# Optimization experiments

Hardware: AMD Instinct MI355X
Metric: run time of the kernel (lower is better)

## Reference

```python
import jax, jax.numpy as jnp
import numpy as np

# Device/group constants for group_idx = 0 (from the source)
V_REF = 0.25
G_MIN = 1.0 / 983.3
G_MAX = 1.0 / 281.3
N_AVG = 2.132
N_STD = 0.095

P, N_IN, N_OUT = 1024, 784, 128


def setup_inputs() -> dict:
    key = jax.random.key(0)
    k1, k2, k3, k4, k5, k6 = jax.random.split(key, 6)
    x = jax.random.uniform(k1, (P, N_IN), dtype=jnp.float32)  # normalized pixel-like inputs in [0,1)
    stdv = 1.0 / np.sqrt(N_IN)
    w_pos = 0.5 + stdv * jax.random.normal(k2, (N_IN, N_OUT), dtype=jnp.float32)
    w_neg = 0.5 + stdv * jax.random.normal(k3, (N_IN, N_OUT), dtype=jnp.float32)
    b_pos = 0.5 * jnp.ones((N_OUT,), dtype=jnp.float32)
    b_neg = 0.5 * jnp.ones((N_OUT,), dtype=jnp.float32)
    # per-device nonlinearity parameter n ~ N(n_avg, n_std), crossbar shape (m, 2*n_out)
    n_param = N_AVG + N_STD * jax.random.normal(k4, (N_IN + 1, 2 * N_OUT), dtype=jnp.float32)
    return {"x": x, "w_pos": w_pos, "w_neg": w_neg, "b_pos": b_pos, "b_neg": b_neg, "n_param": n_param}


def reference(x, w_pos, w_neg, b_pos, b_neg, n_param):
    # --- build combined (weights+bias row), pos/neg column-interleaved crossbar params ---
    cw_pos = jnp.concatenate([w_pos, b_pos[None, :]], axis=0)  # (m, n_out), m = n_in+1
    cw_neg = jnp.concatenate([w_neg, b_neg[None, :]], axis=0)  # (m, n_out)
    m = cw_pos.shape[0]
    weights = jnp.stack([cw_pos, cw_neg], axis=-1).reshape(m, -1)  # (m, 2*n_out), interleaved

    max_weight = jnp.max(jnp.abs(weights))
    # w_params_to_G: linear map of nonnegative weight params onto [G_min, G_max]
    G = G_MIN + (G_MAX - G_MIN) * weights / max_weight  # (m, 2n)

    # x_to_V with appended ones column (bias word line)
    k_V = 2.0 * V_REF
    ones = jnp.ones((x.shape[0], 1), dtype=x.dtype)
    inputs = jnp.concatenate([x, ones], axis=1)  # (p, m)
    V = k_V * inputs  # (p, m)

    # nonlinear IV: I(V) = sign(V) * G*V_ref * n ** log2(|V|/V_ref)
    exponent = jnp.log2(jnp.maximum(jnp.abs(V), 1e-12) / V_REF)  # (p, m)
    I_ind = jnp.sign(V)[:, :, None] * (V_REF * G)[None, :, :] * n_param[None, :, :] ** exponent[:, :, None]  # (p, m, 2n)
    I = jnp.sum(I_ind, axis=1)  # bit-line currents, (p, 2n)

    # I_to_y: differential pos-neg columns, undo conductance/voltage scaling
    I_total = I[:, 0::2] - I[:, 1::2]  # (p, n_out)
    y = I_total * (max_weight / (k_V * (G_MAX - G_MIN)))
    return y
```

## Files before the change

kernel.cpp:

```cpp
#include <hip/hip_runtime.h>
#include <hip/hip_bf16.h>

#define P_ROWS   1024
#define N_IN     784
#define N_OUT    128
#define M_ROWS   785
#define M_PAD    816
#define OUT_ELEMS (P_ROWS * N_OUT)

#define RATIO_F  ((float)((1.0/983.3) / ((1.0/281.3) - (1.0/983.3))))
#define L_AVG_F  1.0922076f
#define LN2_F    0.6931472f

#define NCH      12
#define CHUNK    68
#define NB_MAIN  (64 * NCH)

#define NB_MAX   32

#define PART_OFF 0
#define C_OFF    256

typedef _Float16 half4 __attribute__((ext_vector_type(4)));

__global__ __launch_bounds__(256) void max_reduce(
        const float* __restrict__ wp, const float* __restrict__ wn,
        const float* __restrict__ bp, const float* __restrict__ bn,
        float* __restrict__ partial) {
    const int b = blockIdx.x, t = threadIdx.x;
    const int nW = N_IN * N_OUT;
    int gid = b * 256 + t;
    float v = 0.0f;
    if (gid < N_OUT) v = fmaxf(fabsf(bp[gid]), fabsf(bn[gid]));
    for (int i = gid; i < nW; i += NB_MAX * 256)
        v = fmaxf(v, fmaxf(fabsf(wp[i]), fabsf(wn[i])));
    for (int off = 32; off > 0; off >>= 1)
        v = fmaxf(v, __shfl_down(v, off, 64));
    __shared__ float smax[4];
    if ((t & 63) == 0) smax[t >> 6] = v;
    __syncthreads();
    if (t == 0)
        partial[b] = fmaxf(fmaxf(smax[0], smax[1]), fmaxf(smax[2], smax[3]));
}

__global__ __launch_bounds__(256) void precompute_c(
        const float* __restrict__ wp, const float* __restrict__ wn,
        const float* __restrict__ bp, const float* __restrict__ bn,
        const float* __restrict__ np, const float* __restrict__ partial,
        half4* __restrict__ C) {
    float mw = 0.0f;
    #pragma unroll
    for (int i = 0; i < NB_MAX; ++i) mw = fmaxf(mw, partial[i]);
    const float c0 = 0.5f * RATIO_F * mw;

    int idx = blockIdx.x * 256 + threadIdx.x;
    int m = idx >> 7, k = idx & 127;
    half4 c = {0.0f16, 0.0f16, 0.0f16, 0.0f16};
    if (m < M_ROWS) {
        float wpv = (m < N_IN) ? wp[m * N_OUT + k] : bp[k];
        float wnv = (m < N_IN) ? wn[m * N_OUT + k] : bn[k];
        float npv = np[m * (2 * N_OUT) + 2 * k];
        float nnv = np[m * (2 * N_OUT) + 2 * k + 1];
        float Dp = LN2_F * (__builtin_amdgcn_logf(npv) - L_AVG_F);
        float Dn = LN2_F * (__builtin_amdgcn_logf(nnv) - L_AVG_F);
        float Ap = c0 + 0.5f * wpv;
        float An = c0 + 0.5f * wnv;
        float ApD = Ap * Dp, AnD = An * Dn;
        float ApD2 = ApD * Dp, AnD2 = AnD * Dn;
        float ApD3 = ApD2 * Dp, AnD3 = AnD2 * Dn;
        c.x = (_Float16)(Ap - An);
        c.y = (_Float16)(ApD - AnD);
        c.z = (_Float16)((ApD2 - AnD2) * 0.5f);
        c.w = (_Float16)((ApD3 - AnD3) * (1.0f / 6.0f));
    }
    C[idx] = c;
}

__global__ __launch_bounds__(256) void memristor_main(
        const float* __restrict__ x, const half4* __restrict__ C,
        float* __restrict__ out) {
    const int bid = blockIdx.x;
    const int ch  = bid % NCH;
    const int pb  = bid / NCH;
    const int p0  = pb * 16;
    const int m0  = ch * CHUNK;
    const int t   = threadIdx.x;

    __shared__ __align__(16) float4 F_lds[16 * CHUNK];
    for (int idx = t; idx < 16 * CHUNK; idx += 256) {
        const int r  = idx / CHUNK;
        const int mm = idx - r * CHUNK;
        const int m  = m0 + mm;
        float e;
        if (m < N_IN) {
            float xv = x[(size_t)(p0 + r) * N_IN + m];
            e = (xv > 0.0f) ? __builtin_amdgcn_logf(2.0f * xv) : -1.0e4f;
        } else {
            e = (m == N_IN) ? 1.0f : -1.0e4f;
        }
        float F0 = __builtin_amdgcn_exp2f(e * L_AVG_F);
        float F1 = F0 * e;
        float F2 = F1 * e;
        float F3 = F2 * e;
        F_lds[r * CHUNK + mm] = make_float4(F0, F1, F2, F3);
    }
    __syncthreads();

    const int lane = t & 63;
    const int wid  = t >> 6;
    const int kh   = wid & 1;
    const int pg   = wid >> 1;
    const int k    = kh * 64 + lane;

    const half4*  __restrict__ Cp = C + (size_t)m0 * N_OUT + k;
    const float4* __restrict__ Fb = F_lds + pg * 8 * CHUNK;

    float acc[8];
    #pragma unroll
    for (int i = 0; i < 8; ++i) acc[i] = 0.0f;

    #pragma unroll 2
    for (int mm = 0; mm < CHUNK; ++mm) {
        half4 ch4 = Cp[(size_t)mm * N_OUT];
        float c0 = (float)ch4.x, c1 = (float)ch4.y;
        float c2 = (float)ch4.z, c3 = (float)ch4.w;
        #pragma unroll
        for (int i = 0; i < 8; ++i) {
            float4 f = Fb[i * CHUNK + mm];
            acc[i] = fmaf(f.x, c0,
                     fmaf(f.y, c1,
                     fmaf(f.z, c2,
                     fmaf(f.w, c3, acc[i]))));
        }
    }

    float* o = out + (size_t)(p0 + pg * 8) * N_OUT + k;
    #pragma unroll
    for (int i = 0; i < 8; ++i)
        unsafeAtomicAdd(o + (size_t)i * N_OUT, acc[i]);
}

extern "C" void kernel_launch(void* const* d_in, const int* in_sizes, int n_in,
                              void* d_out, int out_size, void* d_ws, size_t ws_size,
                              hipStream_t stream) {
    const float* x  = (const float*)d_in[0];
    const float* wp = (const float*)d_in[1];
    const float* wn = (const float*)d_in[2];
    const float* bp = (const float*)d_in[3];
    const float* bn = (const float*)d_in[4];
    const float* np = (const float*)d_in[5];
    float* out = (float*)d_out;

    float* partial = (float*)((char*)d_ws + PART_OFF);
    half4* C       = (half4*)((char*)d_ws + C_OFF);

    hipMemsetAsync(out, 0, (size_t)OUT_ELEMS * sizeof(float), stream);
    max_reduce<<<NB_MAX, 256, 0, stream>>>(wp, wn, bp, bn, partial);
    precompute_c<<<(M_PAD * N_OUT) / 256, 256, 0, stream>>>(wp, wn, bp, bn, np, partial, C);
    memristor_main<<<NB_MAIN, 256, 0, stream>>>(x, C, out);
}
```

Before: 93.47 us.

## Store F terms in fp16 LDS and use packed fdot2 with 32-row tiles

```diff
diff --git a/kernel.cpp b/kernel.cpp
--- a/kernel.cpp
+++ b/kernel.cpp
@@ -12,28 +12,46 @@
 #define L_AVG_F  1.0922076f
 #define LN2_F    0.6931472f
 
-#define NCH      12
-#define CHUNK    68
-#define NB_MAIN  (64 * NCH)
+#define NCH      24
+#define CHUNK    34
+#define NB_MAIN  ((P_ROWS / 32) * NCH)
 
 #define NB_MAX   32
 
 #define PART_OFF 0
 #define C_OFF    256
 
-typedef _Float16 half4 __attribute__((ext_vector_type(4)));
+typedef _Float16 half2v __attribute__((ext_vector_type(2)));
+typedef _Float16 half4v __attribute__((ext_vector_type(4)));
+
+__device__ __forceinline__ float fdot2(half2v a, half2v b, float c) {
+#if __has_builtin(__builtin_amdgcn_fdot2)
+    return __builtin_amdgcn_fdot2(a, b, c, false);
+#else
+    return fmaf((float)a.x, (float)b.x, fmaf((float)a.y, (float)b.y, c));
+#endif
+}
 
 __global__ __launch_bounds__(256) void max_reduce(
         const float* __restrict__ wp, const float* __restrict__ wn,
         const float* __restrict__ bp, const float* __restrict__ bn,
         float* __restrict__ partial) {
     const int b = blockIdx.x, t = threadIdx.x;
-    const int nW = N_IN * N_OUT;
+    const int nW4 = (N_IN * N_OUT) / 4;
+    const float4* wp4 = (const float4*)wp;
+    const float4* wn4 = (const float4*)wn;
     int gid = b * 256 + t;
     float v = 0.0f;
-    if (gid < N_OUT) v = fmaxf(fabsf(bp[gid]), fabsf(bn[gid]));
-    for (int i = gid; i < nW; i += NB_MAX * 256)
-        v = fmaxf(v, fmaxf(fabsf(wp[i]), fabsf(wn[i])));
+    if (gid < N_OUT / 4) {
+        float4 a = ((const float4*)bp)[gid], c = ((const float4*)bn)[gid];
+        v = fmaxf(fmaxf(fmaxf(fabsf(a.x), fabsf(a.y)), fmaxf(fabsf(a.z), fabsf(a.w))),
+                  fmaxf(fmaxf(fabsf(c.x), fabsf(c.y)), fmaxf(fabsf(c.z), fabsf(c.w))));
+    }
+    for (int i = gid; i < nW4; i += NB_MAX * 256) {
+        float4 a = wp4[i], c = wn4[i];
+        v = fmaxf(v, fmaxf(fmaxf(fabsf(a.x), fabsf(a.y)), fmaxf(fabsf(a.z), fabsf(a.w))));
+        v = fmaxf(v, fmaxf(fmaxf(fabsf(c.x), fabsf(c.y)), fmaxf(fabsf(c.z), fabsf(c.w))));
+    }
     for (int off = 32; off > 0; off >>= 1)
         v = fmaxf(v, __shfl_down(v, off, 64));
     __shared__ float smax[4];
@@ -47,7 +65,7 @@
         const float* __restrict__ wp, const float* __restrict__ wn,
         const float* __restrict__ bp, const float* __restrict__ bn,
         const float* __restrict__ np, const float* __restrict__ partial,
-        half4* __restrict__ C) {
+        half4v* __restrict__ C) {
     float mw = 0.0f;
     #pragma unroll
     for (int i = 0; i < NB_MAX; ++i) mw = fmaxf(mw, partial[i]);
@@ -55,7 +73,7 @@
 
     int idx = blockIdx.x * 256 + threadIdx.x;
     int m = idx >> 7, k = idx & 127;
-    half4 c = {0.0f16, 0.0f16, 0.0f16, 0.0f16};
+    half4v c = {0.0f16, 0.0f16, 0.0f16, 0.0f16};
     if (m < M_ROWS) {
         float wpv = (m < N_IN) ? wp[m * N_OUT + k] : bp[k];
         float wnv = (m < N_IN) ? wn[m * N_OUT + k] : bn[k];
@@ -65,7 +83,7 @@
         float Dn = LN2_F * (__builtin_amdgcn_logf(nnv) - L_AVG_F);
         float Ap = c0 + 0.5f * wpv;
         float An = c0 + 0.5f * wnv;
-        float ApD = Ap * Dp, AnD = An * Dn;
+        float ApD = Ap * Dp,   AnD = An * Dn;
         float ApD2 = ApD * Dp, AnD2 = AnD * Dn;
         float ApD3 = ApD2 * Dp, AnD3 = AnD2 * Dn;
         c.x = (_Float16)(Ap - An);
@@ -77,17 +95,17 @@
 }
 
 __global__ __launch_bounds__(256) void memristor_main(
-        const float* __restrict__ x, const half4* __restrict__ C,
+        const float* __restrict__ x, const half4v* __restrict__ C,
         float* __restrict__ out) {
     const int bid = blockIdx.x;
     const int ch  = bid % NCH;
     const int pb  = bid / NCH;
-    const int p0  = pb * 16;
+    const int p0  = pb * 32;
     const int m0  = ch * CHUNK;
     const int t   = threadIdx.x;
 
-    __shared__ __align__(16) float4 F_lds[16 * CHUNK];
-    for (int idx = t; idx < 16 * CHUNK; idx += 256) {
+    __shared__ half4v F_lds[32][CHUNK];
+    for (int idx = t; idx < 32 * CHUNK; idx += 256) {
         const int r  = idx / CHUNK;
         const int mm = idx - r * CHUNK;
         const int m  = m0 + mm;
@@ -102,42 +120,42 @@
         float F1 = F0 * e;
         float F2 = F1 * e;
         float F3 = F2 * e;
-        F_lds[r * CHUNK + mm] = make_float4(F0, F1, F2, F3);
+        half4v f = {(_Float16)F0, (_Float16)F1, (_Float16)F2, (_Float16)F3};
+        F_lds[r][mm] = f;
     }
     __syncthreads();
 
     const int lane = t & 63;
-    const int wid  = t >> 6;
-    const int kh   = wid & 1;
-    const int pg   = wid >> 1;
-    const int k    = kh * 64 + lane;
+    const int pg   = t >> 6;
+    const int k    = lane;
 
-    const half4*  __restrict__ Cp = C + (size_t)m0 * N_OUT + k;
-    const float4* __restrict__ Fb = F_lds + pg * 8 * CHUNK;
+    const half4v* __restrict__ Cp = C + (size_t)m0 * N_OUT + k;
+    const half4v* __restrict__ Fb = &F_lds[pg * 8][0];
 
-    float acc[8];
+    float acc[16];
     #pragma unroll
-    for (int i = 0; i < 8; ++i) acc[i] = 0.0f;
+    for (int i = 0; i < 16; ++i) acc[i] = 0.0f;
 
-    #pragma unroll 2
     for (int mm = 0; mm < CHUNK; ++mm) {
-        half4 ch4 = Cp[(size_t)mm * N_OUT];
-        float c0 = (float)ch4.x, c1 = (float)ch4.y;
-        float c2 = (float)ch4.z, c3 = (float)ch4.w;
+        half4v c0 = Cp[(size_t)mm * N_OUT];
+        half4v c1 = Cp[(size_t)mm * N_OUT + 64];
+        half2v c0a = {c0.x, c0.y}, c0b = {c0.z, c0.w};
+        half2v c1a = {c1.x, c1.y}, c1b = {c1.z, c1.w};
         #pragma unroll
         for (int i = 0; i < 8; ++i) {
-            float4 f = Fb[i * CHUNK + mm];
-            acc[i] = fmaf(f.x, c0,
-                     fmaf(f.y, c1,
-                     fmaf(f.z, c2,
-                     fmaf(f.w, c3, acc[i]))));
+            half4v f = Fb[i * CHUNK + mm];
+            half2v fa = {f.x, f.y}, fb = {f.z, f.w};
+            acc[2 * i]     = fdot2(fa, c0a, fdot2(fb, c0b, acc[2 * i]));
+            acc[2 * i + 1] = fdot2(fa, c1a, fdot2(fb, c1b, acc[2 * i + 1]));
         }
     }
 
     float* o = out + (size_t)(p0 + pg * 8) * N_OUT + k;
     #pragma unroll
-    for (int i = 0; i < 8; ++i)
-        unsafeAtomicAdd(o + (size_t)i * N_OUT, acc[i]);
+    for (int i = 0; i < 8; ++i) {
+        unsafeAtomicAdd(o + (size_t)i * N_OUT,      acc[2 * i]);
+        unsafeAtomicAdd(o + (size_t)i * N_OUT + 64, acc[2 * i + 1]);
+    }
 }
 
 extern "C" void kernel_launch(void* const* d_in, const int* in_sizes, int n_in,
@@ -151,8 +169,8 @@
     const float* np = (const float*)d_in[5];
     float* out = (float*)d_out;
 
-    float* partial = (float*)((char*)d_ws + PART_OFF);
-    half4* C       = (half4*)((char*)d_ws + C_OFF);
+    float*  partial = (float*)((char*)d_ws + PART_OFF);
+    half4v* C       = (half4v*)((char*)d_ws + C_OFF);
 
     hipMemsetAsync(out, 0, (size_t)OUT_ELEMS * sizeof(float), stream);
     max_reduce<<<NB_MAX, 256, 0, stream>>>(wp, wn, bp, bn, partial);
```

New measurement: 89.62 us. 1.04x faster.
